# Kernel optimization log

Hardware: AMD Instinct MI355X
Metric: run time of the kernel (lower is better)

Reference implementation:

```python
import jax, jax.numpy as jnp
import numpy as np

D_MODEL = 768
NUM_HEADS = 12
D_K = D_MODEL // NUM_HEADS
D_FF = 2048
LN_EPS = 1e-3  # Keras LayerNormalization default
B, S = 4, 2048


def layer_norm(x, gamma, beta):
    mu = jnp.mean(x, axis=-1, keepdims=True)
    var = jnp.var(x, axis=-1, keepdims=True)
    return (x - mu) * jax.lax.rsqrt(var + LN_EPS) * gamma + beta


def setup_inputs() -> dict:
    key = jax.random.key(0)
    ks = jax.random.split(key, 16)
    sd = 0.02
    inp = {
        "x": jax.random.normal(ks[0], (B, S, D_MODEL), dtype=jnp.float32),
        "src_mask": jnp.zeros((B, 1, 1, S), dtype=jnp.float32),
        "Wq": jax.random.normal(ks[1], (D_MODEL, D_MODEL), jnp.float32) * sd,
        "bq": jnp.zeros((D_MODEL,), jnp.float32),
        "Wk": jax.random.normal(ks[2], (D_MODEL, D_MODEL), jnp.float32) * sd,
        "bk": jnp.zeros((D_MODEL,), jnp.float32),
        "Wv": jax.random.normal(ks[3], (D_MODEL, D_MODEL), jnp.float32) * sd,
        "bv": jnp.zeros((D_MODEL,), jnp.float32),
        "Wo": jax.random.normal(ks[4], (D_MODEL, D_MODEL), jnp.float32) * sd,
        "bo": jnp.zeros((D_MODEL,), jnp.float32),
        "W1": jax.random.normal(ks[5], (D_MODEL, D_FF), jnp.float32) * sd,
        "b1": jnp.zeros((D_FF,), jnp.float32),
        "W2": jax.random.normal(ks[6], (D_FF, D_MODEL), jnp.float32) * sd,
        "b2": jnp.zeros((D_MODEL,), jnp.float32),
        "gamma1": jnp.ones((D_MODEL,), jnp.float32),
        "beta1": jnp.zeros((D_MODEL,), jnp.float32),
        "gamma2": jnp.ones((D_MODEL,), jnp.float32),
        "beta2": jnp.zeros((D_MODEL,), jnp.float32),
    }
    return inp


def encoder_layer(x, src_mask, Wq, bq, Wk, bk, Wv, bv, Wo, bo, W1, b1, W2, b2,
                  gamma1, beta1, gamma2, beta2):
    b, s, _ = x.shape
    def heads(t):  # [B,S,D] -> [B,H,S,Dk]
        return t.reshape(b, s, NUM_HEADS, D_K).transpose(0, 2, 1, 3)
    Q = heads(x @ Wq + bq)
    K = heads(x @ Wk + bk)
    V = heads(x @ Wv + bv)
    scores = jnp.einsum("bhqd,bhkd->bhqk", Q, K) / jnp.sqrt(jnp.float32(D_K))
    scores = scores + src_mask * (-1e9)
    probs = jax.nn.softmax(scores, axis=-1)
    attn = jnp.einsum("bhqk,bhkd->bhqd", probs, V)
    attn = attn.transpose(0, 2, 1, 3).reshape(b, s, D_MODEL)
    attn_out = attn @ Wo + bo
    # dropout is identity at inference
    x1 = layer_norm(x + attn_out, gamma1, beta1)
    ff = jax.nn.relu(x1 @ W1 + b1) @ W2 + b2
    return layer_norm(x1 + ff, gamma2, beta2)


def reference(x, src_mask, Wq, bq, Wk, bk, Wv, bv, Wo, bo, W1, b1, W2, b2,
              gamma1, beta1, gamma2, beta2):
    return encoder_layer(x, src_mask, Wq, bq, Wk, bk, Wv, bv, Wo, bo,
                         W1, b1, W2, b2, gamma1, beta1, gamma2, beta2)
```

## Files before the change

### kernel.cpp

```cpp
#include <hip/hip_runtime.h>


typedef unsigned short u16;
typedef __bf16 bf16x8 __attribute__((ext_vector_type(8)));
typedef __bf16 bf16x4 __attribute__((ext_vector_type(4)));
typedef unsigned short u16x8 __attribute__((ext_vector_type(8)));
typedef float f32x4 __attribute__((ext_vector_type(4)));

#define D_MODEL 768
#define D_FF    2048
#define NH      12
#define DK      64
#define S_LEN   2048
#define M_TOK   8192

#define QSCALE   0.18033688011112042f
#define MSCALE  -1.4426950408889634e9f

__device__ __forceinline__ float bf2f(u16 v) {
    union { unsigned u; float f; } c; c.u = ((unsigned)v) << 16; return c.f;
}
__device__ __forceinline__ void st_bf(u16* p, float v) { *(__bf16*)p = (__bf16)v; }

__device__ __forceinline__ void gload_lds16(const void* g, void* l) {
    __builtin_amdgcn_global_load_lds(
        (const __attribute__((address_space(1))) void*)g,
        (__attribute__((address_space(3))) void*)l, 16, 0, 0);
}

__global__ __launch_bounds__(256)
void prep_k(const float* __restrict__ x, const float* __restrict__ Wq,
            const float* __restrict__ Wk, const float* __restrict__ Wv,
            const float* __restrict__ Wo, const float* __restrict__ W1,
            const float* __restrict__ W2, u16* __restrict__ xb,
            u16* __restrict__ WqkvT, u16* __restrict__ WoT,
            u16* __restrict__ W1T, u16* __restrict__ W2T) {
    __shared__ float t[32][33];
    const int id = blockIdx.x, tid = threadIdx.x;
    if (id >= 5376) {
        const int i = ((id - 5376) * 256 + tid) * 4;
        const float4 v = *(const float4*)(x + i);
        __bf16 o[4] = {(__bf16)v.x, (__bf16)v.y, (__bf16)v.z, (__bf16)v.w};
        *(bf16x4*)(xb + i) = *(bf16x4*)o;
        return;
    }
    const float* in; u16* out; int R, C, bx, by;
    if (id < 2304) {
        const int z = id / 576, r = id % 576;
        in = z == 0 ? Wq : (z == 1 ? Wk : (z == 2 ? Wv : Wo));
        out = z == 3 ? WoT : WqkvT + z * 768 * 768;
        R = 768; C = 768; bx = (r % 24) * 32; by = (r / 24) * 32;
    } else if (id < 3840) {
        const int r = id - 2304;
        in = W1; out = W1T; R = 768; C = 2048;
        bx = (r % 64) * 32; by = (r / 64) * 32;
    } else {
        const int r = id - 3840;
        in = W2; out = W2T; R = 2048; C = 768;
        bx = (r % 24) * 32; by = (r / 24) * 32;
    }
    const int tx = tid & 31, ty = tid >> 5;
#pragma unroll
    for (int i = 0; i < 32; i += 8)
        t[ty + i][tx] = in[(size_t)(by + ty + i) * C + bx + tx];
    __syncthreads();
#pragma unroll
    for (int i = 0; i < 32; i += 8)
        st_bf(&out[(size_t)(bx + ty + i) * R + by + tx], t[tx][ty + i]);
}

__global__ __launch_bounds__(256, 3)
void qkv_gemm_k(const u16* __restrict__ A, const u16* __restrict__ Bt,
                const float* __restrict__ bq, const float* __restrict__ bk,
                const float* __restrict__ bv, u16* __restrict__ Qb,
                u16* __restrict__ Kb, u16* __restrict__ Vt) {
    __shared__ __align__(16) u16 As[2][128 * 32];
    __shared__ __align__(16) u16 Bs[2][128 * 32];
    const int tid = threadIdx.x;
    const int lane = tid & 63, w = tid >> 6;
    const int r16 = lane & 15, qd = lane >> 4;
    const int m0 = blockIdx.x * 128, n0 = blockIdx.y * 128;
    const int wm = (w & 1) << 6, wn = (w >> 1) << 6;
    const int K = D_MODEL;

    f32x4 acc[4][4] = {};

    const u16* aP[2]; const u16* bP[2]; int f8[2];
#pragma unroll
    for (int it = 0; it < 2; ++it) {
        const int f = it * 256 + tid;
        const int row = f >> 2, kc = (f & 3) << 3;
        aP[it] = A  + (size_t)(m0 + row) * K + kc;
        bP[it] = Bt + (size_t)(n0 + row) * K + kc;
        f8[it] = f * 8;
    }

    for (int k0 = 0; k0 < K; k0 += 64) {
#pragma unroll
        for (int p = 0; p < 2; ++p)
#pragma unroll
            for (int it = 0; it < 2; ++it) {
                gload_lds16(aP[it] + k0 + p * 32, &As[p][f8[it]]);
                gload_lds16(bP[it] + k0 + p * 32, &Bs[p][f8[it]]);
            }
        __syncthreads();
#pragma unroll
        for (int p = 0; p < 2; ++p) {
            bf16x8 af[4], bfr[4];
#pragma unroll
            for (int i = 0; i < 4; ++i) {
                af[i]  = *(const bf16x8*)&As[p][(wm + i * 16 + r16) * 32 + qd * 8];
                bfr[i] = *(const bf16x8*)&Bs[p][(wn + i * 16 + r16) * 32 + qd * 8];
            }
#pragma unroll
            for (int i = 0; i < 4; ++i)
#pragma unroll
                for (int j = 0; j < 4; ++j)
                    acc[i][j] = __builtin_amdgcn_mfma_f32_16x16x32_bf16(af[i], bfr[j], acc[i][j], 0, 0, 0);
        }
        __syncthreads();
    }

    const int sel = n0 < 768 ? 0 : (n0 < 1536 ? 1 : 2);
    const float* bias = sel == 0 ? bq : (sel == 1 ? bk : bv);
    const float scale = sel == 0 ? QSCALE : 1.0f;
    const int nbase = n0 - sel * 768;

#pragma unroll
    for (int j = 0; j < 4; ++j) {
        const int ncol = nbase + wn + j * 16 + r16;
        const float bvv = bias[ncol];
#pragma unroll
        for (int i = 0; i < 4; ++i) {
            if (sel == 2) {
                const int h = ncol >> 6, d = ncol & 63;
                const int mb = m0 + wm + i * 16 + qd * 4;
                const int bb = mb >> 11, npb = mb & 2047;
                __bf16 pk[4];
#pragma unroll
                for (int rr = 0; rr < 4; ++rr) pk[rr] = (__bf16)(acc[i][j][rr] + bvv);
                *(bf16x4*)&Vt[(((size_t)(bb * NH + h)) * DK + d) * S_LEN + npb] = *(bf16x4*)pk;
            } else {
#pragma unroll
                for (int rr = 0; rr < 4; ++rr) {
                    const int m = m0 + wm + i * 16 + qd * 4 + rr;
                    const float v = (acc[i][j][rr] + bvv) * scale;
                    if (sel == 0) st_bf(&Qb[(size_t)m * D_MODEL + ncol], v);
                    else          st_bf(&Kb[(size_t)m * D_MODEL + ncol], v);
                }
            }
        }
    }
}

__global__ __launch_bounds__(256, 3)
void gemm_bt_k(const u16* __restrict__ A, const u16* __restrict__ Bt,
               const float* __restrict__ bias, u16* __restrict__ Cout,
               int M, int N, int K, int mode) {
    __shared__ __align__(16) u16 As[2][128 * 32];
    __shared__ __align__(16) u16 Bs[2][128 * 32];
    const int tid = threadIdx.x;
    const int lane = tid & 63, w = tid >> 6;
    const int r16 = lane & 15, qd = lane >> 4;
    const int m0 = blockIdx.x * 128, n0 = blockIdx.y * 128;
    const int wm = (w & 1) << 6, wn = (w >> 1) << 6;

    f32x4 acc[4][4] = {};

    const u16* aP[2]; const u16* bP[2]; int f8[2];
#pragma unroll
    for (int it = 0; it < 2; ++it) {
        const int f = it * 256 + tid;
        const int row = f >> 2, kc = (f & 3) << 3;
        aP[it] = A  + (size_t)(m0 + row) * K + kc;
        bP[it] = Bt + (size_t)(n0 + row) * K + kc;
        f8[it] = f * 8;
    }

    for (int k0 = 0; k0 < K; k0 += 64) {
#pragma unroll
        for (int p = 0; p < 2; ++p)
#pragma unroll
            for (int it = 0; it < 2; ++it) {
                gload_lds16(aP[it] + k0 + p * 32, &As[p][f8[it]]);
                gload_lds16(bP[it] + k0 + p * 32, &Bs[p][f8[it]]);
            }
        __syncthreads();
#pragma unroll
        for (int p = 0; p < 2; ++p) {
            bf16x8 af[4], bfr[4];
#pragma unroll
            for (int i = 0; i < 4; ++i) {
                af[i]  = *(const bf16x8*)&As[p][(wm + i * 16 + r16) * 32 + qd * 8];
                bfr[i] = *(const bf16x8*)&Bs[p][(wn + i * 16 + r16) * 32 + qd * 8];
            }
#pragma unroll
            for (int i = 0; i < 4; ++i)
#pragma unroll
                for (int j = 0; j < 4; ++j)
                    acc[i][j] = __builtin_amdgcn_mfma_f32_16x16x32_bf16(af[i], bfr[j], acc[i][j], 0, 0, 0);
        }
        __syncthreads();
    }

#pragma unroll
    for (int j = 0; j < 4; ++j) {
        const int n = n0 + wn + j * 16 + r16;
        const float bv = bias ? bias[n] : 0.0f;
#pragma unroll
        for (int i = 0; i < 4; ++i) {
#pragma unroll
            for (int rr = 0; rr < 4; ++rr) {
                const int m = m0 + wm + i * 16 + qd * 4 + rr;
                float v = acc[i][j][rr] + bv;
                if (mode == 2) v = fmaxf(v, 0.0f);
                st_bf(&Cout[(size_t)m * N + n], v);
            }
        }
    }
}

__global__ __launch_bounds__(256, 3)
void gemm_bt64_k(const u16* __restrict__ A, const u16* __restrict__ Bt,
                 const float* __restrict__ bias, u16* __restrict__ Cout,
                 int M, int N, int K, int mode) {
    __shared__ __align__(16) u16 As[2][64 * 32];
    __shared__ __align__(16) u16 Bs[2][128 * 32];
    const int tid = threadIdx.x;
    const int lane = tid & 63, w = tid >> 6;
    const int r16 = lane & 15, qd = lane >> 4;
    const int m0 = blockIdx.x * 64, n0 = blockIdx.y * 128;
    const int wm = (w & 1) << 5, wn = (w >> 1) << 6;

    f32x4 acc[2][4] = {};

    const int arow = tid >> 2, akc = (tid & 3) << 3;
    const u16* aP = A + (size_t)(m0 + arow) * K + akc;
    const u16* bP[2]; int f8[2];
#pragma unroll
    for (int it = 0; it < 2; ++it) {
        const int f = it * 256 + tid;
        const int row = f >> 2, kc = (f & 3) << 3;
        bP[it] = Bt + (size_t)(n0 + row) * K + kc;
        f8[it] = f * 8;
    }

    for (int k0 = 0; k0 < K; k0 += 64) {
#pragma unroll
        for (int p = 0; p < 2; ++p) {
            gload_lds16(aP + k0 + p * 32, &As[p][tid * 8]);
#pragma unroll
            for (int it = 0; it < 2; ++it)
                gload_lds16(bP[it] + k0 + p * 32, &Bs[p][f8[it]]);
        }
        __syncthreads();
#pragma unroll
        for (int p = 0; p < 2; ++p) {
            bf16x8 af[2], bfr[4];
#pragma unroll
            for (int i = 0; i < 2; ++i)
                af[i] = *(const bf16x8*)&As[p][(wm + i * 16 + r16) * 32 + qd * 8];
#pragma unroll
            for (int j = 0; j < 4; ++j)
                bfr[j] = *(const bf16x8*)&Bs[p][(wn + j * 16 + r16) * 32 + qd * 8];
#pragma unroll
            for (int i = 0; i < 2; ++i)
#pragma unroll
                for (int j = 0; j < 4; ++j)
                    acc[i][j] = __builtin_amdgcn_mfma_f32_16x16x32_bf16(af[i], bfr[j], acc[i][j], 0, 0, 0);
        }
        __syncthreads();
    }

#pragma unroll
    for (int j = 0; j < 4; ++j) {
        const int n = n0 + wn + j * 16 + r16;
        const float bv = bias ? bias[n] : 0.0f;
#pragma unroll
        for (int i = 0; i < 2; ++i) {
#pragma unroll
            for (int rr = 0; rr < 4; ++rr) {
                const int m = m0 + wm + i * 16 + qd * 4 + rr;
                float v = acc[i][j][rr] + bv;
                if (mode == 2) v = fmaxf(v, 0.0f);
                st_bf(&Cout[(size_t)m * N + n], v);
            }
        }
    }
}

#define TS 72

__global__ __launch_bounds__(256, 3)
void attn_k(const u16* __restrict__ Qg, const u16* __restrict__ Kg,
            const u16* __restrict__ Vtg, const float* __restrict__ maskg,
            u16* __restrict__ Og) {
    const int tid = threadIdx.x, lane = tid & 63, w = tid >> 6;
    const int qh = w & 1, kh = w >> 1;
    const int r16 = lane & 15, qd = lane >> 4;
    const int q0 = blockIdx.x * 128;
    const int h = blockIdx.y, b = blockIdx.z;

    __shared__ __align__(16) u16 sm[(64 + 64 + 128) * TS];
    u16* Ks  = sm;
    u16* Vts = sm + 64 * TS;
    u16* Ps  = sm + 128 * TS;

    bf16x8 qa[4][2];
#pragma unroll
    for (int mt = 0; mt < 4; ++mt)
#pragma unroll
        for (int ks = 0; ks < 2; ++ks)
            qa[mt][ks] = *(const bf16x8*)(Qg +
                ((size_t)((b * S_LEN + q0 + qh * 64 + mt * 16 + r16) * NH + h)) * DK +
                ks * 32 + qd * 8);

    const int srow = tid >> 3, sc = (tid & 7) << 3;
    const u16* vsrc = Vtg + (((size_t)(b * NH + h)) * DK) * S_LEN;
    u16x8 kreg[2], vreg[2];
#pragma unroll
    for (int it = 0; it < 2; ++it) {
        const int row = srow + it * 32;
        kreg[it] = *(const u16x8*)(Kg + ((size_t)((b * S_LEN + row) * NH + h)) * DK + sc);
        vreg[it] = *(const u16x8*)(vsrc + (size_t)row * S_LEN + sc);
    }

    float l_i[4] = {0.0f, 0.0f, 0.0f, 0.0f};
    f32x4 Oacc[4][4] = {};

    for (int kt = 0; kt < S_LEN / 64; ++kt) {
        const int ks0 = kt * 64;

#pragma unroll
        for (int it = 0; it < 2; ++it) {
            const int row = srow + it * 32;
            *(u16x8*)&Ks[row * TS + sc]  = kreg[it];
            *(u16x8*)&Vts[row * TS + sc] = vreg[it];
        }

        float4 mrow[2];
#pragma unroll
        for (int nt = 0; nt < 2; ++nt) {
            const float4 mm = ((const float4*)(maskg + (size_t)b * S_LEN + ks0))[kh * 8 + nt * 4 + qd];
            mrow[nt].x = mm.x * MSCALE; mrow[nt].y = mm.y * MSCALE;
            mrow[nt].z = mm.z * MSCALE; mrow[nt].w = mm.w * MSCALE;
        }
        __syncthreads();

        f32x4 sa[4][2];
#pragma unroll
        for (int mt = 0; mt < 4; ++mt)
#pragma unroll
            for (int nt = 0; nt < 2; ++nt) {
                sa[mt][nt][0] = mrow[nt].x; sa[mt][nt][1] = mrow[nt].y;
                sa[mt][nt][2] = mrow[nt].z; sa[mt][nt][3] = mrow[nt].w;
            }
#pragma unroll
        for (int ks = 0; ks < 2; ++ks) {
            bf16x8 kb[2];
#pragma unroll
            for (int nt = 0; nt < 2; ++nt)
                kb[nt] = *(const bf16x8*)&Ks[(kh * 32 + nt * 16 + r16) * TS + ks * 32 + qd * 8];
#pragma unroll
            for (int mt = 0; mt < 4; ++mt)
#pragma unroll
                for (int nt = 0; nt < 2; ++nt)
                    sa[mt][nt] = __builtin_amdgcn_mfma_f32_16x16x32_bf16(kb[nt], qa[mt][ks], sa[mt][nt], 0, 0, 0);
        }

#pragma unroll
        for (int mt = 0; mt < 4; ++mt) {
            float rsum = 0.0f;
#pragma unroll
            for (int nt = 0; nt < 2; ++nt) {
                sa[mt][nt][0] = __builtin_amdgcn_exp2f(sa[mt][nt][0]);
                sa[mt][nt][1] = __builtin_amdgcn_exp2f(sa[mt][nt][1]);
                sa[mt][nt][2] = __builtin_amdgcn_exp2f(sa[mt][nt][2]);
                sa[mt][nt][3] = __builtin_amdgcn_exp2f(sa[mt][nt][3]);
                rsum += sa[mt][nt][0] + sa[mt][nt][1] + sa[mt][nt][2] + sa[mt][nt][3];
            }
            rsum += __shfl_xor(rsum, 16);
            rsum += __shfl_xor(rsum, 32);
            l_i[mt] += rsum;
        }

#pragma unroll
        for (int mt = 0; mt < 4; ++mt)
#pragma unroll
            for (int nt = 0; nt < 2; ++nt) {
                __bf16 pk[4];
#pragma unroll
                for (int rr = 0; rr < 4; ++rr) pk[rr] = (__bf16)sa[mt][nt][rr];
                *(bf16x4*)&Ps[(qh * 64 + mt * 16 + r16) * TS + kh * 32 + nt * 16 + qd * 4] = *(bf16x4*)pk;
            }

        if (kt + 1 < S_LEN / 64) {
            const int ns0 = ks0 + 64;
#pragma unroll
            for (int it = 0; it < 2; ++it) {
                const int row = srow + it * 32;
                kreg[it] = *(const u16x8*)(Kg + ((size_t)((b * S_LEN + ns0 + row) * NH + h)) * DK + sc);
                vreg[it] = *(const u16x8*)(vsrc + (size_t)row * S_LEN + ns0 + sc);
            }
        }

        {
            bf16x8 pa[4], vb[4];
#pragma unroll
            for (int mt = 0; mt < 4; ++mt)
                pa[mt] = *(const bf16x8*)&Ps[(qh * 64 + mt * 16 + r16) * TS + kh * 32 + qd * 8];
#pragma unroll
            for (int vt = 0; vt < 4; ++vt)
                vb[vt] = *(const bf16x8*)&Vts[(vt * 16 + r16) * TS + kh * 32 + qd * 8];
#pragma unroll
            for (int mt = 0; mt < 4; ++mt)
#pragma unroll
                for (int vt = 0; vt < 4; ++vt)
                    Oacc[mt][vt] = __builtin_amdgcn_mfma_f32_16x16x32_bf16(pa[mt], vb[vt], Oacc[mt][vt], 0, 0, 0);
        }
        __syncthreads();
    }

    __syncthreads();
    float* mb  = (float*)sm;
    float* lsm = mb + 128 * 64;
    if (kh == 0) {
#pragma unroll
        for (int mt = 0; mt < 4; ++mt) {
            if (qd == 0) lsm[(qh * 4 + mt) * 16 + r16] = l_i[mt];
#pragma unroll
            for (int vt = 0; vt < 4; ++vt)
#pragma unroll
                for (int rr = 0; rr < 4; ++rr)
                    mb[(qh * 64 + mt * 16 + qd * 4 + rr) * 64 + vt * 16 + r16] = Oacc[mt][vt][rr];
        }
    }
    __syncthreads();
    if (kh == 1) {
#pragma unroll
        for (int mt = 0; mt < 4; ++mt) {
            const float linv = 1.0f / (l_i[mt] + lsm[(qh * 4 + mt) * 16 + r16]);
#pragma unroll
            for (int rr = 0; rr < 4; ++rr) {
                const float lr = __shfl(linv, qd * 4 + rr);
                const int qrow = q0 + qh * 64 + mt * 16 + qd * 4 + rr;
#pragma unroll
                for (int vt = 0; vt < 4; ++vt) {
                    const float o = Oacc[mt][vt][rr] +
                        mb[(qh * 64 + mt * 16 + qd * 4 + rr) * 64 + vt * 16 + r16];
                    st_bf(&Og[((size_t)((b * S_LEN + qrow) * NH + h)) * DK + vt * 16 + r16],
                          o * lr);
                }
            }
        }
    }
}

__global__ __launch_bounds__(256, 4)
void resln_k(const u16* __restrict__ xb, const u16* __restrict__ yb,
             const float* __restrict__ gamma, const float* __restrict__ beta,
             u16* __restrict__ outb, float* __restrict__ outf) {
    const int row = blockIdx.x, tid = threadIdx.x;
    const int lane = tid & 63, w = tid >> 6;
    __shared__ float redS[4], redS2[4];
    const size_t base = (size_t)row * D_MODEL;
    float h[3], s = 0.0f, s2 = 0.0f;
#pragma unroll
    for (int i = 0; i < 3; ++i) {
        const int c = i * 256 + tid;
        const float v = bf2f(xb[base + c]) + bf2f(yb[base + c]);
        h[i] = v; s += v; s2 += v * v;
    }
#pragma unroll
    for (int off = 32; off >= 1; off >>= 1) { s += __shfl_xor(s, off); s2 += __shfl_xor(s2, off); }
    if (lane == 0) { redS[w] = s; redS2[w] = s2; }
    __syncthreads();
    s  = redS[0] + redS[1] + redS[2] + redS[3];
    s2 = redS2[0] + redS2[1] + redS2[2] + redS2[3];
    const float mu  = s * (1.0f / D_MODEL);
    const float var = s2 * (1.0f / D_MODEL) - mu * mu;
    const float rstd = rsqrtf(var + 1e-3f);
#pragma unroll
    for (int i = 0; i < 3; ++i) {
        const int c = i * 256 + tid;
        const float o = (h[i] - mu) * rstd * gamma[c] + beta[c];
        if (outb) st_bf(&outb[base + c], o);
        if (outf) outf[base + c] = o;
    }
}

extern "C" void kernel_launch(void* const* d_in, const int* in_sizes, int n_in,
                              void* d_out, int out_size, void* d_ws, size_t ws_size,
                              hipStream_t stream) {
    (void)in_sizes; (void)n_in; (void)out_size; (void)ws_size;
    const float* x    = (const float*)d_in[0];
    const float* mask = (const float*)d_in[1];
    const float* Wq = (const float*)d_in[2];  const float* bq  = (const float*)d_in[3];
    const float* Wk = (const float*)d_in[4];  const float* bk  = (const float*)d_in[5];
    const float* Wv = (const float*)d_in[6];  const float* bv  = (const float*)d_in[7];
    const float* Wo = (const float*)d_in[8];  const float* bo  = (const float*)d_in[9];
    const float* W1 = (const float*)d_in[10]; const float* b1  = (const float*)d_in[11];
    const float* W2 = (const float*)d_in[12]; const float* b2  = (const float*)d_in[13];
    const float* g1 = (const float*)d_in[14]; const float* be1 = (const float*)d_in[15];
    const float* g2 = (const float*)d_in[16]; const float* be2 = (const float*)d_in[17];

    char* ws = (char*)d_ws;
    u16* xb     = (u16*)(ws + 0);
    u16* WqkvT  = (u16*)(ws + 12582912);
    u16* WoT    = (u16*)(ws + 16121856);
    u16* W1T    = (u16*)(ws + 17301504);
    u16* W2T    = (u16*)(ws + 20447232);
    u16* Qb     = (u16*)(ws + 23592960);
    u16* Kb     = (u16*)(ws + 36175872);
    u16* Vtg    = (u16*)(ws + 48758784);
    u16* Ab     = (u16*)(ws + 61341696);
    u16* Yb     = (u16*)(ws + 73924608);
    u16* X1b    = (u16*)(ws + 86507520);
    u16* H1b    = (u16*)(ws + 23592960);
    u16* Y2b    = (u16*)(ws + 73924608);

    const dim3 blk(256);

    prep_k<<<dim3(11520), blk, 0, stream>>>(x, Wq, Wk, Wv, Wo, W1, W2,
                                            xb, WqkvT, WoT, W1T, W2T);

    qkv_gemm_k<<<dim3(64, 18), blk, 0, stream>>>(xb, WqkvT, bq, bk, bv, Qb, Kb, Vtg);

    attn_k<<<dim3(16, NH, 4), blk, 0, stream>>>(Qb, Kb, Vtg, mask, Ab);

    gemm_bt64_k<<<dim3(128, 6), blk, 0, stream>>>(Ab, WoT, bo, Yb, M_TOK, D_MODEL, D_MODEL, 1);

    resln_k<<<dim3(M_TOK), blk, 0, stream>>>(xb, Yb, g1, be1, X1b, nullptr);

    gemm_bt_k<<<dim3(64, 16), blk, 0, stream>>>(X1b, W1T, b1, H1b, M_TOK, D_FF, D_MODEL, 2);

    gemm_bt64_k<<<dim3(128, 6), blk, 0, stream>>>(H1b, W2T, b2, Y2b, M_TOK, D_MODEL, D_FF, 1);

    resln_k<<<dim3(M_TOK), blk, 0, stream>>>(X1b, Y2b, g2, be2, nullptr, (float*)d_out);
}
```

Measured before the change: 352.7 us.

## Replace FF1 GEMM with 256x256-tile 8-wave kernel using interleaved prefetch

Replaces the generic 128x128 GEMM for the first feed-forward layer with a dedicated kernel using 256x256 tiles, 512 threads and a double-buffered 64 KB LDS stage. Loads for the next K-tile are split into four chunks interleaved between MFMA phases, with s_setprio raised around the MFMA bursts. The operand order is swapped so each lane writes four contiguous bf16 outputs in the epilogue. The intent is more data reuse per LDS load and better overlap of global loads with compute. The cost is only 256 blocks, so a larger share of the GPU's CUs may sit idle or tail effects may grow, and register pressure rises.

```diff
diff --git a/kernel.cpp b/kernel.cpp
--- a/kernel.cpp
+++ b/kernel.cpp
@@ -154,73 +154,6 @@
 }
 
 __global__ __launch_bounds__(256, 3)
-void gemm_bt_k(const u16* __restrict__ A, const u16* __restrict__ Bt,
-               const float* __restrict__ bias, u16* __restrict__ Cout,
-               int M, int N, int K, int mode) {
-    __shared__ __align__(16) u16 As[2][128 * 32];
-    __shared__ __align__(16) u16 Bs[2][128 * 32];
-    const int tid = threadIdx.x;
-    const int lane = tid & 63, w = tid >> 6;
-    const int r16 = lane & 15, qd = lane >> 4;
-    const int m0 = blockIdx.x * 128, n0 = blockIdx.y * 128;
-    const int wm = (w & 1) << 6, wn = (w >> 1) << 6;
-
-    f32x4 acc[4][4] = {};
-
-    const u16* aP[2]; const u16* bP[2]; int f8[2];
-#pragma unroll
-    for (int it = 0; it < 2; ++it) {
-        const int f = it * 256 + tid;
-        const int row = f >> 2, kc = (f & 3) << 3;
-        aP[it] = A  + (size_t)(m0 + row) * K + kc;
-        bP[it] = Bt + (size_t)(n0 + row) * K + kc;
-        f8[it] = f * 8;
-    }
-
-    for (int k0 = 0; k0 < K; k0 += 64) {
-#pragma unroll
-        for (int p = 0; p < 2; ++p)
-#pragma unroll
-            for (int it = 0; it < 2; ++it) {
-                gload_lds16(aP[it] + k0 + p * 32, &As[p][f8[it]]);
-                gload_lds16(bP[it] + k0 + p * 32, &Bs[p][f8[it]]);
-            }
-        __syncthreads();
-#pragma unroll
-        for (int p = 0; p < 2; ++p) {
-            bf16x8 af[4], bfr[4];
-#pragma unroll
-            for (int i = 0; i < 4; ++i) {
-                af[i]  = *(const bf16x8*)&As[p][(wm + i * 16 + r16) * 32 + qd * 8];
-                bfr[i] = *(const bf16x8*)&Bs[p][(wn + i * 16 + r16) * 32 + qd * 8];
-            }
-#pragma unroll
-            for (int i = 0; i < 4; ++i)
-#pragma unroll
-                for (int j = 0; j < 4; ++j)
-                    acc[i][j] = __builtin_amdgcn_mfma_f32_16x16x32_bf16(af[i], bfr[j], acc[i][j], 0, 0, 0);
-        }
-        __syncthreads();
-    }
-
-#pragma unroll
-    for (int j = 0; j < 4; ++j) {
-        const int n = n0 + wn + j * 16 + r16;
-        const float bv = bias ? bias[n] : 0.0f;
-#pragma unroll
-        for (int i = 0; i < 4; ++i) {
-#pragma unroll
-            for (int rr = 0; rr < 4; ++rr) {
-                const int m = m0 + wm + i * 16 + qd * 4 + rr;
-                float v = acc[i][j][rr] + bv;
-                if (mode == 2) v = fmaxf(v, 0.0f);
-                st_bf(&Cout[(size_t)m * N + n], v);
-            }
-        }
-    }
-}
-
-__global__ __launch_bounds__(256, 3)
 void gemm_bt64_k(const u16* __restrict__ A, const u16* __restrict__ Bt,
                  const float* __restrict__ bias, u16* __restrict__ Cout,
                  int M, int N, int K, int mode) {
@@ -285,6 +218,147 @@
                 if (mode == 2) v = fmaxf(v, 0.0f);
                 st_bf(&Cout[(size_t)m * N + n], v);
             }
+        }
+    }
+}
+
+__global__ __launch_bounds__(512, 2)
+void ff1_k(const u16* __restrict__ A, const u16* __restrict__ Bt,
+           const float* __restrict__ bias, u16* __restrict__ C) {
+    __shared__ __align__(16) u16 AB[2][32768];
+    const int tid = threadIdx.x, lane = tid & 63;
+    const int w = tid >> 6;
+    const int wm2 = w >> 2, wn4 = w & 3;
+    const int r16 = lane & 15, qd = lane >> 4;
+    const int m0 = blockIdx.x * 256, n0 = blockIdx.y * 256;
+    const int K = D_MODEL, NT = 12;
+
+    const u16* aS[4]; const u16* bS[4];
+#pragma unroll
+    for (int l = 0; l < 4; ++l) {
+        const int f = l * 512 + tid;
+        const int row = (f >> 2) & 255, ks = f >> 10, e = (f & 3) << 3;
+        aS[l] = A  + (size_t)(m0 + row) * K + ks * 32 + e;
+        bS[l] = Bt + (size_t)(n0 + row) * K + ks * 32 + e;
+    }
+
+#pragma unroll
+    for (int l = 0; l < 4; ++l) {
+        gload_lds16(aS[l], &AB[0][(l * 512 + tid) * 8]);
+        gload_lds16(bS[l], &AB[0][16384 + (l * 512 + tid) * 8]);
+    }
+    asm volatile("s_waitcnt vmcnt(0)" ::: "memory");
+    __builtin_amdgcn_s_barrier();
+
+    f32x4 acc[8][4] = {};
+    bf16x8 af[4][2], bfr[4][2];
+    const int arow0 = wm2 * 128 + r16;
+    const int brow0 = wn4 * 64 + r16;
+
+    for (int t = 0; t < NT; ++t) {
+        const int cur = t & 1, nxt = cur ^ 1;
+        const u16* ab = AB[cur];
+        const int ka = (t + 1) * 64;
+        const bool more = (t + 1) < NT;
+
+#pragma unroll
+        for (int mt = 0; mt < 4; ++mt)
+#pragma unroll
+            for (int ks = 0; ks < 2; ++ks)
+                af[mt][ks] = *(const bf16x8*)&ab[ks * 8192 + (arow0 + mt * 16) * 32 + qd * 8];
+#pragma unroll
+        for (int nt = 0; nt < 2; ++nt)
+#pragma unroll
+            for (int ks = 0; ks < 2; ++ks)
+                bfr[nt][ks] = *(const bf16x8*)&ab[16384 + ks * 8192 + (brow0 + nt * 16) * 32 + qd * 8];
+        if (more) {
+            gload_lds16(aS[0] + ka, &AB[nxt][(0 * 512 + tid) * 8]);
+            gload_lds16(aS[1] + ka, &AB[nxt][(1 * 512 + tid) * 8]);
+        }
+        __builtin_amdgcn_s_setprio(1);
+#pragma unroll
+        for (int mt = 0; mt < 4; ++mt)
+#pragma unroll
+            for (int nt = 0; nt < 2; ++nt)
+#pragma unroll
+                for (int ks = 0; ks < 2; ++ks)
+                    acc[mt][nt] = __builtin_amdgcn_mfma_f32_16x16x32_bf16(bfr[nt][ks], af[mt][ks], acc[mt][nt], 0, 0, 0);
+        __builtin_amdgcn_s_setprio(0);
+        __builtin_amdgcn_s_barrier();
+
+#pragma unroll
+        for (int nt = 2; nt < 4; ++nt)
+#pragma unroll
+            for (int ks = 0; ks < 2; ++ks)
+                bfr[nt][ks] = *(const bf16x8*)&ab[16384 + ks * 8192 + (brow0 + nt * 16) * 32 + qd * 8];
+        if (more) {
+            gload_lds16(aS[2] + ka, &AB[nxt][(2 * 512 + tid) * 8]);
+            gload_lds16(aS[3] + ka, &AB[nxt][(3 * 512 + tid) * 8]);
+        }
+        __builtin_amdgcn_s_setprio(1);
+#pragma unroll
+        for (int mt = 0; mt < 4; ++mt)
+#pragma unroll
+            for (int nt = 2; nt < 4; ++nt)
+#pragma unroll
+                for (int ks = 0; ks < 2; ++ks)
+                    acc[mt][nt] = __builtin_amdgcn_mfma_f32_16x16x32_bf16(bfr[nt][ks], af[mt][ks], acc[mt][nt], 0, 0, 0);
+        __builtin_amdgcn_s_setprio(0);
+        __builtin_amdgcn_s_barrier();
+
+#pragma unroll
+        for (int mt = 0; mt < 4; ++mt)
+#pragma unroll
+            for (int ks = 0; ks < 2; ++ks)
+                af[mt][ks] = *(const bf16x8*)&ab[ks * 8192 + (arow0 + 64 + mt * 16) * 32 + qd * 8];
+        if (more) {
+            gload_lds16(bS[0] + ka, &AB[nxt][16384 + (0 * 512 + tid) * 8]);
+            gload_lds16(bS[1] + ka, &AB[nxt][16384 + (1 * 512 + tid) * 8]);
+        }
+        __builtin_amdgcn_s_setprio(1);
+#pragma unroll
+        for (int mt = 0; mt < 4; ++mt)
+#pragma unroll
+            for (int nt = 0; nt < 2; ++nt)
+#pragma unroll
+                for (int ks = 0; ks < 2; ++ks)
+                    acc[4 + mt][nt] = __builtin_amdgcn_mfma_f32_16x16x32_bf16(bfr[nt][ks], af[mt][ks], acc[4 + mt][nt], 0, 0, 0);
+        __builtin_amdgcn_s_setprio(0);
+        __builtin_amdgcn_s_barrier();
+
+        if (more) {
+            gload_lds16(bS[2] + ka, &AB[nxt][16384 + (2 * 512 + tid) * 8]);
+            gload_lds16(bS[3] + ka, &AB[nxt][16384 + (3 * 512 + tid) * 8]);
+        }
+        __builtin_amdgcn_s_setprio(1);
+#pragma unroll
+        for (int mt = 0; mt < 4; ++mt)
+#pragma unroll
+            for (int nt = 2; nt < 4; ++nt)
+#pragma unroll
+                for (int ks = 0; ks < 2; ++ks)
+                    acc[4 + mt][nt] = __builtin_amdgcn_mfma_f32_16x16x32_bf16(bfr[nt][ks], af[mt][ks], acc[4 + mt][nt], 0, 0, 0);
+        __builtin_amdgcn_s_setprio(0);
+
+        if (more) {
+            asm volatile("s_waitcnt vmcnt(0)" ::: "memory");
+            __builtin_amdgcn_s_barrier();
+        }
+    }
+
+#pragma unroll
+    for (int nt = 0; nt < 4; ++nt) {
+        const int nb = n0 + wn4 * 64 + nt * 16 + qd * 4;
+        const float4 bv = *(const float4*)&bias[nb];
+        const float b4[4] = {bv.x, bv.y, bv.z, bv.w};
+#pragma unroll
+        for (int mi = 0; mi < 8; ++mi) {
+            const int m = m0 + wm2 * 128 + (mi >> 2) * 64 + (mi & 3) * 16 + r16;
+            __bf16 pk[4];
+#pragma unroll
+            for (int rr = 0; rr < 4; ++rr)
+                pk[rr] = (__bf16)fmaxf(acc[mi][nt][rr] + b4[rr], 0.0f);
+            *(bf16x4*)&C[(size_t)m * D_FF + nb] = *(bf16x4*)pk;
         }
     }
 }
@@ -532,7 +606,7 @@
 
     resln_k<<<dim3(M_TOK), blk, 0, stream>>>(xb, Yb, g1, be1, X1b, nullptr);
 
-    gemm_bt_k<<<dim3(64, 16), blk, 0, stream>>>(X1b, W1T, b1, H1b, M_TOK, D_FF, D_MODEL, 2);
+    ff1_k<<<dim3(32, 8), dim3(512), 0, stream>>>(X1b, W1T, b1, H1b);
 
     gemm_bt64_k<<<dim3(128, 6), blk, 0, stream>>>(H1b, W2T, b2, Y2b, M_TOK, D_MODEL, D_FF, 1);
 
```

After: 345.4 us. 1.02x faster.
